# Performance work log

Hardware: AMD Instinct MI355X
Metric: run time of the kernel (lower is better)

Reference implementation:

```python
import jax, jax.numpy as jnp
import numpy as np

SIG = 10
C = 0.0
STD = 1.0
N_ATOMS = 21
N_TRAIN = 8192
DESC = N_ATOMS * (N_ATOMS - 1) // 2  # 210
M = 64


def setup_inputs() -> dict:
    key = jax.random.key(0)
    k1, k2, k3 = jax.random.split(key, 3)
    Rs = jax.random.normal(k1, (M, N_ATOMS, 3), dtype=jnp.float32)
    xs_train = jax.random.uniform(k2, (N_TRAIN, DESC), dtype=jnp.float32)
    Jx_alphas = jax.random.normal(k3, (N_TRAIN, DESC), dtype=jnp.float32)
    return {"Rs": Rs, "xs_train": xs_train, "Jx_alphas": Jx_alphas}


def reference(Rs, xs_train, Jx_alphas):
    sig = SIG
    q = np.sqrt(5.0) / sig
    n = N_ATOMS
    # pairwise atom displacements / distances: [M, n, n, 3], [M, n, n]
    diffs = Rs[:, :, None, :] - Rs[:, None, :, :]
    dists = jnp.linalg.norm(diffs, axis=-1)
    eye = jnp.eye(n, dtype=bool)
    dists = jnp.where(eye, jnp.inf, dists)  # kill diagonal
    i, j = np.tril_indices(n, k=-1)
    xs = 1.0 / dists[:, i, j]                       # [M, D] inverse-distance descriptor
    x_diffs = q * xs[:, None, :] - q * xs_train     # [M, T, D]
    x_dists = jnp.linalg.norm(x_diffs, axis=-1)     # [M, T]
    exp_xs = (5.0 / (3.0 * sig ** 2)) * jnp.exp(-x_dists)
    dot = jnp.einsum('mtd,td->mt', x_diffs, Jx_alphas)
    exp_xs_1 = exp_xs * (1.0 + x_dists)
    F1s_x = jnp.einsum('mt,mtd->md', exp_xs * dot, x_diffs)  # [M, D]
    F2s_x = exp_xs_1 @ Jx_alphas                              # [M, D]
    Fs_x = (F1s_x - F2s_x) * STD
    # expand_tril: scatter D lower-tri values to symmetric [M, n, n], zero diag
    full = jnp.zeros((Fs_x.shape[0], n, n), dtype=Fs_x.dtype)
    full = full.at[:, i, j].set(Fs_x).at[:, j, i].set(Fs_x)
    Fs = jnp.einsum('mab,mabc->mac', full / dists ** 3, diffs)  # diag: 0/inf -> 0
    Es = jnp.sum(exp_xs_1 * dot, axis=-1) / q
    Es = C + Es * STD
    return Es, Fs
```

## Files before the change

kernel.cpp:

```cpp
#include <hip/hip_runtime.h>
#include <math.h>

#define NA   21
#define NM   64
#define ND   210
#define DP   224
#define NT   8192
#define NCH  28
#define KS2  32

#define QC 0.22360679774997896f
#define KE 0.016666666666666666f

typedef short bf8 __attribute__((ext_vector_type(8)));
typedef float f4  __attribute__((ext_vector_type(4)));

#define O_XFT  1835008u
#define O_JFT  2752512u
#define O_W1   3670016u
#define O_E1   3932160u
#define O_AF   4194304u
#define O_QG   4201472u
#define O_NX   4232192u
#define O_PB   4261056u
#define O_ESP  5178560u
#define O_WAP  5211328u

__device__ __forceinline__ unsigned short f2bf(float f) {
    unsigned u = __float_as_uint(f);
    u += 0x7fffu + ((u >> 16) & 1u);
    return (unsigned short)(u >> 16);
}
__device__ __forceinline__ float bf2f(unsigned short h) {
    return __uint_as_float((unsigned)h << 16);
}

__device__ __forceinline__ void d_to_ij(int d, int& i, int& j) {
    int ii = (int)((1.0f + sqrtf(1.0f + 8.0f * (float)d)) * 0.5f);
    while (ii * (ii - 1) / 2 > d) --ii;
    while ((ii + 1) * ii / 2 <= d) ++ii;
    i = ii;
    j = d - ii * (ii - 1) / 2;
}

__global__ __launch_bounds__(256) void k_geom(
    const float* __restrict__ Rs, unsigned short* __restrict__ Af,
    float* __restrict__ qxsG, float* __restrict__ nx) {
    const int m = blockIdx.x, tid = threadIdx.x;
    __shared__ float R[NA * 3];
    __shared__ float red[256];
    if (tid < NA * 3) R[tid] = Rs[m * NA * 3 + tid];
    __syncthreads();
    float local = 0.0f;
    if (tid < DP) {
        float vr = 0.0f;
        unsigned short hv = 0;
        if (tid < ND) {
            int i, j; d_to_ij(tid, i, j);
            float dx = R[i * 3] - R[j * 3];
            float dy = R[i * 3 + 1] - R[j * 3 + 1];
            float dz = R[i * 3 + 2] - R[j * 3 + 2];
            float v = QC / sqrtf(dx * dx + dy * dy + dz * dz);
            hv = f2bf(v);
            vr = bf2f(hv);
        }
        Af[(((m >> 4) * NCH + (tid >> 3)) * 16 + (m & 15)) * 8 + (tid & 7)] = hv;
        qxsG[(tid >> 2) * 256 + m * 4 + (tid & 3)] = vr;
        local = vr * vr;
    }
    red[tid] = local;
    __syncthreads();
    for (int s = 128; s > 0; s >>= 1) {
        if (tid < s) red[tid] += red[tid + s];
        __syncthreads();
    }
    if (tid == 0) nx[m] = red[0];
}

__global__ __launch_bounds__(256) void k_s1p(
    const float* __restrict__ xs, const float* __restrict__ Jx,
    const unsigned short* __restrict__ Af, const float* __restrict__ nxg,
    unsigned short* __restrict__ XfT, unsigned short* __restrict__ JfT,
    unsigned short* __restrict__ w1f, unsigned short* __restrict__ e1f,
    float* __restrict__ EsPart, float* __restrict__ WaPart) {
    const int b = blockIdx.x, tid = threadIdx.x;
    const int lane = tid & 63;
    const int w = tid >> 6;
    const int col = lane & 15, quad = lane >> 4;

    __shared__ unsigned short xJh[2 * 16 * DP];
    __shared__ float Dw[64][17];
    __shared__ float De[64][17];
    __shared__ float ntL[16], cjL[16];
    char* xB = (char*)xJh;

    const unsigned short* ap = Af + ((size_t)(w * NCH + quad) * 16 + col) * 8;
    bf8 af[7];
#pragma unroll
    for (int kc = 0; kc < 7; ++kc) af[kc] = *(const bf8*)(ap + kc * 512);
    float nxv[4];
#pragma unroll
    for (int r = 0; r < 4; ++r) nxv[r] = nxg[w * 16 + quad * 4 + r];

    if (tid < 224) {
        const int arr = tid / 112, rem = tid - arr * 112;
        const int t = rem / 7, k2 = rem - t * 7;
        *(unsigned*)(xB + arr * 7168 +
                     (((unsigned)(t * 448 + 420 + k2 * 4)) ^ ((unsigned)((t & 7) << 4)))) = 0u;
    }
    const float2* sx = (const float2*)(xs + (size_t)b * 16 * ND);
    const float2* sj = (const float2*)(Jx + (size_t)b * 16 * ND);
#pragma unroll
    for (int k = 0; k < 7; ++k) {
        const int p = k * 256 + tid;
        if (p < 1680) {
            const float2 vx = sx[p];
            const float2 vj = sj[p];
            const int t = p / 105;
            const unsigned bo = ((unsigned)(4 * p + 28 * t)) ^ ((unsigned)((t & 7) << 4));
            *(unsigned*)(xB + bo) =
                (unsigned)f2bf(QC * vx.x) | ((unsigned)f2bf(QC * vx.y) << 16);
            *(unsigned*)(xB + 7168 + bo) =
                (unsigned)f2bf(vj.x) | ((unsigned)f2bf(vj.y) << 16);
        }
    }
    __syncthreads();

    {
        const int tt = tid >> 4, l = tid & 15;
        const unsigned swt = (unsigned)((tt & 7) << 4);
        float sn = 0.0f, sc2 = 0.0f;
#pragma unroll
        for (int c = l; c < DP; c += 16) {
            const unsigned off = ((unsigned)(tt * 448 + 2 * c)) ^ swt;
            const float x = bf2f(*(const unsigned short*)(xB + off));
            const float jv = bf2f(*(const unsigned short*)(xB + 7168 + off));
            sn = fmaf(x, x, sn);
            sc2 = fmaf(x, jv, sc2);
        }
#pragma unroll
        for (int o = 1; o < 16; o <<= 1) {
            sn += __shfl_xor(sn, o);
            sc2 += __shfl_xor(sc2, o);
        }
        if (l == 0) { ntL[tt] = sn; cjL[tt] = sc2; }
    }
#pragma unroll
    for (int k = 0; k < 4; ++k) {
        const int idx = k * 256 + tid;
        if (idx < 896) {
            const int arr = idx / 448;
            const int rem = idx - arr * 448;
            const int dtile = rem >> 5;
            const int rem2 = rem & 31;
            const int tql = rem2 >> 4, cc = rem2 & 15;
            const int dbyte = 2 * (dtile * 16 + cc);
            union { unsigned short us[8]; uint4 v; } u;
#pragma unroll
            for (int i = 0; i < 8; ++i) {
                const int t = tql * 8 + i;
                const unsigned off =
                    ((unsigned)(t * 448 + dbyte)) ^ ((unsigned)((t & 7) << 4));
                u.us[i] = *(const unsigned short*)(xB + arr * 7168 + off);
            }
            const size_t o2 = ((size_t)(dtile * 1024 + b * 2 + tql) * 16 + cc) * 8;
            *(uint4*)((arr ? JfT : XfT) + o2) = u.v;
        }
    }
    __syncthreads();

    const unsigned base0 = (unsigned)(col * 448 + quad * 16);
    const unsigned swc = (unsigned)((col & 7) << 4);
    bf8 bx[2], bj[2];
    bx[0] = *(const bf8*)(xB + (base0 ^ swc));
    bj[0] = *(const bf8*)(xB + 7168 + (base0 ^ swc));
    bx[1] = *(const bf8*)(xB + ((base0 + 64) ^ swc));
    bj[1] = *(const bf8*)(xB + 7168 + ((base0 + 64) ^ swc));
    f4 c1 = {0.f, 0.f, 0.f, 0.f};
    f4 c2 = {0.f, 0.f, 0.f, 0.f};
#pragma unroll
    for (int kc = 0; kc < 7; ++kc) {
        const int s = kc & 1;
        c1 = __builtin_amdgcn_mfma_f32_16x16x32_bf16(af[kc], bx[s], c1, 0, 0, 0);
        c2 = __builtin_amdgcn_mfma_f32_16x16x32_bf16(af[kc], bj[s], c2, 0, 0, 0);
        if (kc < 5) {
            bx[s] = *(const bf8*)(xB + ((base0 + (kc + 2) * 64) ^ swc));
            bj[s] = *(const bf8*)(xB + 7168 + ((base0 + (kc + 2) * 64) ^ swc));
        }
    }

    const float ntv = ntL[col], cjv = cjL[col];
    float esA[4], wlA[4];
#pragma unroll
    for (int r = 0; r < 4; ++r) {
        const int m = w * 16 + quad * 4 + r;
        float sq = fmaxf(nxv[r] - 2.0f * c1[r] + ntv, 0.0f);
        float xd = sqrtf(sq);
        float e = KE * expf(-xd);
        float dotv = c2[r] - cjv;
        float wv = e * dotv;
        float ev = e * (1.0f + xd);
        Dw[m][col] = wv;
        De[m][col] = ev;
        esA[r] = ev * dotv;
        wlA[r] = wv;
    }
    __syncthreads();
    {
        const int aidx = tid >> 7;
        const int c = tid & 127;
        const int mtile = c >> 5, tql = (c >> 4) & 1, colm = c & 15;
        const float* srcD = aidx ? &De[0][0] : &Dw[0][0];
        unsigned short* dst = aidx ? e1f : w1f;
        const int m = mtile * 16 + colm;
        union { unsigned short us[8]; uint4 v; } u;
#pragma unroll
        for (int i = 0; i < 8; ++i) u.us[i] = f2bf(srcD[m * 17 + tql * 8 + i]);
        const size_t off = ((size_t)(mtile * 1024 + b * 2 + tql) * 16 + colm) * 8;
        *(uint4*)(dst + off) = u.v;
    }
#pragma unroll
    for (int r = 0; r < 4; ++r) {
        float e = esA[r], wl = wlA[r];
#pragma unroll
        for (int o = 1; o < 16; o <<= 1) {
            e += __shfl_xor(e, o);
            wl += __shfl_xor(wl, o);
        }
        if (col == 0) {
            const int m = w * 16 + quad * 4 + r;
            EsPart[(size_t)m * 512 + b] = e;
            WaPart[(size_t)m * 512 + b] = wl;
        }
    }
}

__global__ __launch_bounds__(256) void k_stage2(
    const unsigned short* __restrict__ w1f, const unsigned short* __restrict__ e1f,
    const unsigned short* __restrict__ XfT, const unsigned short* __restrict__ JfT,
    float* __restrict__ Pbuf) {
    const int tid = threadIdx.x;
    const int lane = tid & 63;
    const int w = tid >> 6;
    const int col = lane & 15, quad = lane >> 4;
    const int dt = blockIdx.x;
    const int by = blockIdx.y;

    const unsigned short* awp = w1f + ((size_t)(w * 1024 + by * 32 + quad) * 16 + col) * 8;
    const unsigned short* aep = e1f + ((size_t)(w * 1024 + by * 32 + quad) * 16 + col) * 8;
    const unsigned short* bxp = XfT + ((size_t)(dt * 1024 + by * 32 + quad) * 16 + col) * 8;
    const unsigned short* bjp = JfT + ((size_t)(dt * 1024 + by * 32 + quad) * 16 + col) * 8;

    bf8 aw[2], ae[2], bx[2], bj[2];
    aw[0] = *(const bf8*)awp;         ae[0] = *(const bf8*)aep;
    bx[0] = *(const bf8*)bxp;         bj[0] = *(const bf8*)bjp;
    aw[1] = *(const bf8*)(awp + 512); ae[1] = *(const bf8*)(aep + 512);
    bx[1] = *(const bf8*)(bxp + 512); bj[1] = *(const bf8*)(bjp + 512);

    f4 dA = {0.f, 0.f, 0.f, 0.f};
    f4 dB = {0.f, 0.f, 0.f, 0.f};
#pragma unroll
    for (int kk = 0; kk < 8; ++kk) {
        const int s = kk & 1;
        dA = __builtin_amdgcn_mfma_f32_16x16x32_bf16(aw[s], bx[s], dA, 0, 0, 0);
        dB = __builtin_amdgcn_mfma_f32_16x16x32_bf16(ae[s], bj[s], dB, 0, 0, 0);
        if (kk < 6) {
            aw[s] = *(const bf8*)(awp + (kk + 2) * 512);
            ae[s] = *(const bf8*)(aep + (kk + 2) * 512);
            bx[s] = *(const bf8*)(bxp + (kk + 2) * 512);
            bj[s] = *(const bf8*)(bjp + (kk + 2) * 512);
        }
    }
    float* p = Pbuf + (size_t)by * 28672 + dt * 16 + col;
#pragma unroll
    for (int r = 0; r < 4; ++r) {
        const int m = w * 16 + quad * 4 + r;
        p[m * DP] = dA[r];
        p[14336 + m * DP] = dB[r];
    }
}

__global__ void k_final(const float* __restrict__ Rs, const float* __restrict__ qxsG,
                        const float* __restrict__ Pbuf, const float* __restrict__ EsPart,
                        const float* __restrict__ WaPart, float* __restrict__ out) {
    int m = blockIdx.x, tid = threadIdx.x;
    __shared__ float R[NA * 3];
    __shared__ float Ff[NA][NA];
    __shared__ float redE[256];
    __shared__ float redW[256];
    __shared__ float ABs[DP];
    if (tid < NA * 3) R[tid] = Rs[m * NA * 3 + tid];
    if (tid < NA) Ff[tid][tid] = 0.0f;
    if (tid < DP) {
        const float* p0 = Pbuf + (size_t)m * DP + tid;
        float s1 = 0.0f, s2 = 0.0f;
#pragma unroll
        for (int ks = 0; ks < KS2; ++ks) {
            s1 += p0[(size_t)ks * 28672];
            s2 += p0[(size_t)ks * 28672 + 14336];
        }
        ABs[tid] = s1 + s2;
    }
    {
        const float2 ep = ((const float2*)(EsPart + (size_t)m * 512))[tid];
        const float2 wp = ((const float2*)(WaPart + (size_t)m * 512))[tid];
        redE[tid] = ep.x + ep.y;
        redW[tid] = wp.x + wp.y;
    }
    __syncthreads();
    for (int s = 128; s > 0; s >>= 1) {
        if (tid < s) {
            redE[tid] += redE[tid + s];
            redW[tid] += redW[tid + s];
        }
        __syncthreads();
    }
    const float Wa = redW[0];
    if (tid < ND) {
        int i, j; d_to_ij(tid, i, j);
        float dx = R[i * 3] - R[j * 3];
        float dy = R[i * 3 + 1] - R[j * 3 + 1];
        float dz = R[i * 3 + 2] - R[j * 3 + 2];
        float dist2 = dx * dx + dy * dy + dz * dz;
        float fsx = qxsG[(tid >> 2) * 256 + m * 4 + (tid & 3)] * Wa - ABs[tid];
        float f = fsx / (dist2 * sqrtf(dist2));
        Ff[i][j] = f;
        Ff[j][i] = f;
    }
    __syncthreads();
    if (tid < NA * 3) {
        int a = tid / 3, c = tid % 3;
        float s = 0.0f;
        for (int b = 0; b < NA; ++b) {
            if (b == a) continue;
            s += Ff[a][b] * (R[a * 3 + c] - R[b * 3 + c]);
        }
        out[NM + m * NA * 3 + tid] = s;
    }
    if (tid == 0) out[m] = redE[0] / QC;
}

extern "C" void kernel_launch(void* const* d_in, const int* in_sizes, int n_in,
                              void* d_out, int out_size, void* d_ws, size_t ws_size,
                              hipStream_t stream) {
    const float* Rs = (const float*)d_in[0];
    const float* xs_train = (const float*)d_in[1];
    const float* Jx_alphas = (const float*)d_in[2];
    float* out = (float*)d_out;
    float* ws = (float*)d_ws;

    unsigned short* XfT = (unsigned short*)(ws + O_XFT);
    unsigned short* JfT = (unsigned short*)(ws + O_JFT);
    unsigned short* w1f = (unsigned short*)(ws + O_W1);
    unsigned short* e1f = (unsigned short*)(ws + O_E1);
    unsigned short* Af  = (unsigned short*)(ws + O_AF);
    float* qxsG   = ws + O_QG;
    float* nx     = ws + O_NX;
    float* Pbuf   = ws + O_PB;
    float* EsPart = ws + O_ESP;
    float* WaPart = ws + O_WAP;

    k_geom<<<NM, 256, 0, stream>>>(Rs, Af, qxsG, nx);
    k_s1p<<<512, 256, 0, stream>>>(xs_train, Jx_alphas, Af, nx, XfT, JfT,
                                   w1f, e1f, EsPart, WaPart);
    k_stage2<<<dim3(14, KS2), 256, 0, stream>>>(w1f, e1f, XfT, JfT, Pbuf);
    k_final<<<NM, 256, 0, stream>>>(Rs, qxsG, Pbuf, EsPart, WaPart, out);
}
```

Before: 90.25 us.

## Fuse geometry kernel into stage-1 and halve stage-2 K-split count

Removes the separate k_geom launch. Each stage-1 block now loads all coordinates into shared memory and recomputes the bf16 inverse-distance A fragments and their norms in registers. k_final recomputes the rounded descriptor itself instead of reading it from a buffer. Stage-2 halves its split-K grid, so each block runs 16 K steps with a 4-deep register prefetch, and k_final sums fewer partials. This trades one launch plus some global traffic for redundant geometry work in all 512 stage-1 blocks and a smaller stage-2 grid.

```diff
diff --git a/kernel.cpp b/kernel.cpp
--- a/kernel.cpp
+++ b/kernel.cpp
@@ -7,7 +7,7 @@
 #define DP   224
 #define NT   8192
 #define NCH  28
-#define KS2  32
+#define KS2  16
 
 #define QC 0.22360679774997896f
 #define KE 0.016666666666666666f
@@ -19,9 +19,6 @@
 #define O_JFT  2752512u
 #define O_W1   3670016u
 #define O_E1   3932160u
-#define O_AF   4194304u
-#define O_QG   4201472u
-#define O_NX   4232192u
 #define O_PB   4261056u
 #define O_ESP  5178560u
 #define O_WAP  5211328u
@@ -43,43 +40,9 @@
     j = d - ii * (ii - 1) / 2;
 }
 
-__global__ __launch_bounds__(256) void k_geom(
-    const float* __restrict__ Rs, unsigned short* __restrict__ Af,
-    float* __restrict__ qxsG, float* __restrict__ nx) {
-    const int m = blockIdx.x, tid = threadIdx.x;
-    __shared__ float R[NA * 3];
-    __shared__ float red[256];
-    if (tid < NA * 3) R[tid] = Rs[m * NA * 3 + tid];
-    __syncthreads();
-    float local = 0.0f;
-    if (tid < DP) {
-        float vr = 0.0f;
-        unsigned short hv = 0;
-        if (tid < ND) {
-            int i, j; d_to_ij(tid, i, j);
-            float dx = R[i * 3] - R[j * 3];
-            float dy = R[i * 3 + 1] - R[j * 3 + 1];
-            float dz = R[i * 3 + 2] - R[j * 3 + 2];
-            float v = QC / sqrtf(dx * dx + dy * dy + dz * dz);
-            hv = f2bf(v);
-            vr = bf2f(hv);
-        }
-        Af[(((m >> 4) * NCH + (tid >> 3)) * 16 + (m & 15)) * 8 + (tid & 7)] = hv;
-        qxsG[(tid >> 2) * 256 + m * 4 + (tid & 3)] = vr;
-        local = vr * vr;
-    }
-    red[tid] = local;
-    __syncthreads();
-    for (int s = 128; s > 0; s >>= 1) {
-        if (tid < s) red[tid] += red[tid + s];
-        __syncthreads();
-    }
-    if (tid == 0) nx[m] = red[0];
-}
-
 __global__ __launch_bounds__(256) void k_s1p(
     const float* __restrict__ xs, const float* __restrict__ Jx,
-    const unsigned short* __restrict__ Af, const float* __restrict__ nxg,
+    const float* __restrict__ Rs,
     unsigned short* __restrict__ XfT, unsigned short* __restrict__ JfT,
     unsigned short* __restrict__ w1f, unsigned short* __restrict__ e1f,
     float* __restrict__ EsPart, float* __restrict__ WaPart) {
@@ -92,15 +55,21 @@
     __shared__ float Dw[64][17];
     __shared__ float De[64][17];
     __shared__ float ntL[16], cjL[16];
+    __shared__ float Rall[NM * NA * 3];
+    __shared__ int   ijL[ND];
+    __shared__ float nxL[NM];
     char* xB = (char*)xJh;
 
-    const unsigned short* ap = Af + ((size_t)(w * NCH + quad) * 16 + col) * 8;
-    bf8 af[7];
-#pragma unroll
-    for (int kc = 0; kc < 7; ++kc) af[kc] = *(const bf8*)(ap + kc * 512);
-    float nxv[4];
-#pragma unroll
-    for (int r = 0; r < 4; ++r) nxv[r] = nxg[w * 16 + quad * 4 + r];
+#pragma unroll
+    for (int k = 0; k < 4; ++k) {
+        const int i4 = k * 256 + tid;
+        if (i4 < 1008) ((float4*)Rall)[i4] = ((const float4*)Rs)[i4];
+    }
+    if (tid < ND) {
+        int i, j; d_to_ij(tid, i, j);
+        ijL[tid] = (i << 8) | j;
+    }
+    __syncthreads();
 
     if (tid < 224) {
         const int arr = tid / 112, rem = tid - arr * 112;
@@ -124,6 +93,32 @@
                 (unsigned)f2bf(vj.x) | ((unsigned)f2bf(vj.y) << 16);
         }
     }
+    const int mA = w * 16 + col;
+    const float* Rm = Rall + mA * 63;
+    bf8 af[7];
+    float nxp = 0.0f;
+#pragma unroll
+    for (int kc = 0; kc < 7; ++kc) {
+#pragma unroll
+        for (int i = 0; i < 8; ++i) {
+            const int d = kc * 32 + quad * 8 + i;
+            unsigned short hv = 0;
+            if (d < ND) {
+                const int pij = ijL[d];
+                const int ai = pij >> 8, aj = pij & 255;
+                const float dx = Rm[ai * 3]     - Rm[aj * 3];
+                const float dy = Rm[ai * 3 + 1] - Rm[aj * 3 + 1];
+                const float dz = Rm[ai * 3 + 2] - Rm[aj * 3 + 2];
+                hv = f2bf(QC / sqrtf(dx * dx + dy * dy + dz * dz));
+            }
+            af[kc][i] = (short)hv;
+            const float vr = bf2f(hv);
+            nxp = fmaf(vr, vr, nxp);
+        }
+    }
+    nxp += __shfl_xor(nxp, 16);
+    nxp += __shfl_xor(nxp, 32);
+    if (quad == 0) nxL[mA] = nxp;
     __syncthreads();
 
     {
@@ -194,7 +189,7 @@
 #pragma unroll
     for (int r = 0; r < 4; ++r) {
         const int m = w * 16 + quad * 4 + r;
-        float sq = fmaxf(nxv[r] - 2.0f * c1[r] + ntv, 0.0f);
+        float sq = fmaxf(nxL[m] - 2.0f * c1[r] + ntv, 0.0f);
         float xd = sqrtf(sq);
         float e = KE * expf(-xd);
         float dotv = c2[r] - cjv;
@@ -246,29 +241,32 @@
     const int dt = blockIdx.x;
     const int by = blockIdx.y;
 
-    const unsigned short* awp = w1f + ((size_t)(w * 1024 + by * 32 + quad) * 16 + col) * 8;
-    const unsigned short* aep = e1f + ((size_t)(w * 1024 + by * 32 + quad) * 16 + col) * 8;
-    const unsigned short* bxp = XfT + ((size_t)(dt * 1024 + by * 32 + quad) * 16 + col) * 8;
-    const unsigned short* bjp = JfT + ((size_t)(dt * 1024 + by * 32 + quad) * 16 + col) * 8;
-
-    bf8 aw[2], ae[2], bx[2], bj[2];
-    aw[0] = *(const bf8*)awp;         ae[0] = *(const bf8*)aep;
-    bx[0] = *(const bf8*)bxp;         bj[0] = *(const bf8*)bjp;
-    aw[1] = *(const bf8*)(awp + 512); ae[1] = *(const bf8*)(aep + 512);
-    bx[1] = *(const bf8*)(bxp + 512); bj[1] = *(const bf8*)(bjp + 512);
+    const unsigned short* awp = w1f + ((size_t)(w * 1024 + by * 64 + quad) * 16 + col) * 8;
+    const unsigned short* aep = e1f + ((size_t)(w * 1024 + by * 64 + quad) * 16 + col) * 8;
+    const unsigned short* bxp = XfT + ((size_t)(dt * 1024 + by * 64 + quad) * 16 + col) * 8;
+    const unsigned short* bjp = JfT + ((size_t)(dt * 1024 + by * 64 + quad) * 16 + col) * 8;
+
+    bf8 aw[4], ae[4], bx[4], bj[4];
+#pragma unroll
+    for (int s = 0; s < 4; ++s) {
+        aw[s] = *(const bf8*)(awp + s * 512);
+        ae[s] = *(const bf8*)(aep + s * 512);
+        bx[s] = *(const bf8*)(bxp + s * 512);
+        bj[s] = *(const bf8*)(bjp + s * 512);
+    }
 
     f4 dA = {0.f, 0.f, 0.f, 0.f};
     f4 dB = {0.f, 0.f, 0.f, 0.f};
 #pragma unroll
-    for (int kk = 0; kk < 8; ++kk) {
-        const int s = kk & 1;
+    for (int kk = 0; kk < 16; ++kk) {
+        const int s = kk & 3;
         dA = __builtin_amdgcn_mfma_f32_16x16x32_bf16(aw[s], bx[s], dA, 0, 0, 0);
         dB = __builtin_amdgcn_mfma_f32_16x16x32_bf16(ae[s], bj[s], dB, 0, 0, 0);
-        if (kk < 6) {
-            aw[s] = *(const bf8*)(awp + (kk + 2) * 512);
-            ae[s] = *(const bf8*)(aep + (kk + 2) * 512);
-            bx[s] = *(const bf8*)(bxp + (kk + 2) * 512);
-            bj[s] = *(const bf8*)(bjp + (kk + 2) * 512);
+        if (kk < 12) {
+            aw[s] = *(const bf8*)(awp + (kk + 4) * 512);
+            ae[s] = *(const bf8*)(aep + (kk + 4) * 512);
+            bx[s] = *(const bf8*)(bxp + (kk + 4) * 512);
+            bj[s] = *(const bf8*)(bjp + (kk + 4) * 512);
         }
     }
     float* p = Pbuf + (size_t)by * 28672 + dt * 16 + col;
@@ -280,7 +278,7 @@
     }
 }
 
-__global__ void k_final(const float* __restrict__ Rs, const float* __restrict__ qxsG,
+__global__ void k_final(const float* __restrict__ Rs,
                         const float* __restrict__ Pbuf, const float* __restrict__ EsPart,
                         const float* __restrict__ WaPart, float* __restrict__ out) {
     int m = blockIdx.x, tid = threadIdx.x;
@@ -322,7 +320,8 @@
         float dy = R[i * 3 + 1] - R[j * 3 + 1];
         float dz = R[i * 3 + 2] - R[j * 3 + 2];
         float dist2 = dx * dx + dy * dy + dz * dz;
-        float fsx = qxsG[(tid >> 2) * 256 + m * 4 + (tid & 3)] * Wa - ABs[tid];
+        float qxs = bf2f(f2bf(QC / sqrtf(dist2)));
+        float fsx = qxs * Wa - ABs[tid];
         float f = fsx / (dist2 * sqrtf(dist2));
         Ff[i][j] = f;
         Ff[j][i] = f;
@@ -353,16 +352,12 @@
     unsigned short* JfT = (unsigned short*)(ws + O_JFT);
     unsigned short* w1f = (unsigned short*)(ws + O_W1);
     unsigned short* e1f = (unsigned short*)(ws + O_E1);
-    unsigned short* Af  = (unsigned short*)(ws + O_AF);
-    float* qxsG   = ws + O_QG;
-    float* nx     = ws + O_NX;
     float* Pbuf   = ws + O_PB;
     float* EsPart = ws + O_ESP;
     float* WaPart = ws + O_WAP;
 
-    k_geom<<<NM, 256, 0, stream>>>(Rs, Af, qxsG, nx);
-    k_s1p<<<512, 256, 0, stream>>>(xs_train, Jx_alphas, Af, nx, XfT, JfT,
+    k_s1p<<<512, 256, 0, stream>>>(xs_train, Jx_alphas, Rs, XfT, JfT,
                                    w1f, e1f, EsPart, WaPart);
     k_stage2<<<dim3(14, KS2), 256, 0, stream>>>(w1f, e1f, XfT, JfT, Pbuf);
-    k_final<<<NM, 256, 0, stream>>>(Rs, qxsG, Pbuf, EsPart, WaPart, out);
-}
+    k_final<<<NM, 256, 0, stream>>>(Rs, Pbuf, EsPart, WaPart, out);
+}
```

Result: slower. 107.1 us (+18.7%).
